# Optimization experiments

Hardware: AMD Instinct MI355X
Metric: run time of the kernel (lower is better)

Reference implementation:

```python
import jax, jax.numpy as jnp
import numpy as np
import math

B, N, CS, CZ, H, C, P, PV, NB = 1, 512, 384, 128, 12, 16, 4, 8, 64


def quat_to_rot(q):
    q = q / jnp.clip(jnp.linalg.norm(q, axis=-1, keepdims=True), 1e-8)
    w, x, y, z = q[..., 0], q[..., 1], q[..., 2], q[..., 3]
    return jnp.stack([
        w*w + x*x - y*y - z*z, 2*(x*y - w*z), 2*(x*z + w*y),
        2*(x*y + w*z), w*w - x*x + y*y - z*z, 2*(y*z - w*x),
        2*(x*z - w*y), 2*(y*z + w*x), w*w - x*x - y*y + z*z,
    ], axis=-1).reshape(q.shape[:-1] + (3, 3))


def setup_inputs() -> dict:
    key = jax.random.key(0)
    ks = jax.random.split(key, 28)
    def n(k, shape, sc=1.0):
        return jax.random.normal(k, shape, jnp.float32) * sc
    s = n(ks[0], (B, N, CS))
    z = n(ks[1], (B, N, N, CZ))
    translations = n(ks[2], (B, N, 3)) * 4.0  # spread distances over 0-32A bins
    rotations = quat_to_rot(n(ks[3], (B, N, 4)))  # valid SO(3) frames
    mask = jnp.ones((B, N), dtype=bool)
    inv = lambda fan: 1.0 / math.sqrt(fan)
    return {
        's': s, 'z': z, 'translations': translations, 'rotations': rotations, 'mask': mask,
        'Wq': n(ks[4], (CS, H*C), inv(CS)), 'bq': n(ks[5], (H*C,), 0.01),
        'Wk': n(ks[6], (CS, H*C), inv(CS)), 'bk': n(ks[7], (H*C,), 0.01),
        'Wv': n(ks[8], (CS, H*C), inv(CS)), 'bv': n(ks[9], (H*C,), 0.01),
        'Wqp': n(ks[10], (CS, H*P*3), inv(CS)), 'bqp': n(ks[11], (H*P*3,), 0.01),
        'Wkp': n(ks[12], (CS, H*P*3), inv(CS)), 'bkp': n(ks[13], (H*P*3,), 0.01),
        'Wvp': n(ks[14], (CS, H*PV*3), inv(CS)), 'bvp': n(ks[15], (H*PV*3,), 0.01),
        'Wb': n(ks[16], (CZ, H), inv(CZ)), 'bb': n(ks[17], (H,), 0.01),
        'dist_emb': n(ks[18], (NB, H), 0.02),
        'scale_logits': n(ks[19], (3, H), 0.1),
        'head_weights': jnp.abs(n(ks[20], (H,))) * 0.2 + 0.8,
        'Wout': n(ks[21], (H*(C + PV*4 + CZ), CS), inv(H*(C + PV*4 + CZ))),
        'bout': n(ks[22], (CS,), 0.01),
    }


def reference(s, z, translations, rotations, mask, Wq, bq, Wk, bk, Wv, bv,
              Wqp, bqp, Wkp, bkp, Wvp, bvp, Wb, bb, dist_emb, scale_logits,
              head_weights, Wout, bout):
    b, n, _ = s.shape
    q = (s @ Wq + bq).reshape(b, n, H, C)
    k = (s @ Wk + bk).reshape(b, n, H, C)
    v = (s @ Wv + bv).reshape(b, n, H, C)
    q_pts = (s @ Wqp + bqp).reshape(b, n, H, P, 3)
    k_pts = (s @ Wkp + bkp).reshape(b, n, H, P, 3)
    v_pts = (s @ Wvp + bvp).reshape(b, n, H, PV, 3)
    t = translations[:, :, None, None, :]
    q_g = jnp.einsum('bnij,bnhpj->bnhpi', rotations, q_pts) + t
    k_g = jnp.einsum('bnij,bnhpj->bnhpi', rotations, k_pts) + t
    v_g = jnp.einsum('bnij,bnhpj->bnhpi', rotations, v_pts) + t
    scalar_logits = jnp.einsum('bnhc,bmhc->bnmh', q, k) / math.sqrt(C)
    # squared point distances, summed over points p and coords i, via expansion
    q_sq = (q_g**2).sum((-1, -2))  # (b, n, h)
    k_sq = (k_g**2).sum((-1, -2))
    cross = jnp.einsum('bnhpi,bmhpi->bnmh', q_g, k_g)
    point_dist = q_sq[:, :, None, :] + k_sq[:, None, :, :] - 2.0 * cross
    point_logits = -0.5 * point_dist * head_weights
    pair_bias = z @ Wb + bb  # (b, n, m, h)
    pair_dist = jnp.linalg.norm(
        translations[:, :, None, :] - translations[:, None, :, :], axis=-1)
    edges = jnp.linspace(0.0, 32.0, NB + 1)
    bins = jnp.clip(jnp.searchsorted(edges, pair_dist, side='left') - 1, 0, NB - 1)
    dist_bias = dist_emb[bins]
    local = (pair_dist <= 5.0).astype(s.dtype)
    medium = ((pair_dist > 5.0) & (pair_dist <= 15.0)).astype(s.dtype)
    scales = jnp.stack([local, medium, jnp.ones_like(pair_dist)], axis=-1)
    per_head = jax.nn.softmax(scale_logits, axis=0)  # (3, h)
    multiscale = jnp.einsum('bnms,sh->bnmh', scales, per_head)
    logits = scalar_logits + point_logits + pair_bias + dist_bias + multiscale
    m2d = mask[:, :, None] & mask[:, None, :]
    logits = jnp.where(m2d[..., None], logits, -10000.0)
    attn = jax.nn.softmax(logits.astype(jnp.float32), axis=2).astype(s.dtype)
    out_scalar = jnp.einsum('bnmh,bmhc->bnhc', attn, v)
    out_pts_g = jnp.einsum('bnmh,bmhpi->bnhpi', attn, v_g)
    out_pts_l = jnp.einsum('bnji,bnhpj->bnhpi', rotations, out_pts_g - t)  # R^T x
    out_norms = jnp.linalg.norm(out_pts_l, axis=-1)  # (b, n, h, pv)
    pair_feat = jnp.einsum('bnmh,bnmc->bnhc', attn, z)
    feats = jnp.concatenate(
        [out_scalar, out_pts_l.reshape(b, n, H, PV * 3), out_norms, pair_feat],
        axis=-1).reshape(b, n, -1)
    return feats @ Wout + bout
```

## Files before the change

kernel.cpp:

```cpp
#include <hip/hip_runtime.h>
#include <math.h>

#define N   512
#define CS  384
#define CZ  128
#define H   12
#define C   16
#define P   4
#define PV  8
#define NB  64
#define KSP 528
#define QKD 28
#define QPAD 68
#define APAD 516
#define ZP2 132

#define OFF_Q    0
#define OFF_K    98304
#define OFF_V    196608
#define OFF_QP   294912
#define OFF_KP   368640
#define OFF_VP   442368
#define OFF_QG   589824
#define OFF_KG   663552
#define OFF_VG   737280
#define OFF_QSQ  884736
#define OFF_KSQ  890880
#define OFF_LOG  897024
#define OFF_FEAT 4042752

__global__ __launch_bounds__(256) void k_proj(
    const float* __restrict__ s,
    const float* __restrict__ Wq,  const float* __restrict__ bq,
    const float* __restrict__ Wk,  const float* __restrict__ bk,
    const float* __restrict__ Wv,  const float* __restrict__ bv,
    const float* __restrict__ Wqp, const float* __restrict__ bqp,
    const float* __restrict__ Wkp, const float* __restrict__ bkp,
    const float* __restrict__ Wvp, const float* __restrict__ bvp,
    float* __restrict__ ws)
{
    __shared__ float s_s[16*388];
    __shared__ float part[4*16*68];
    const int tid = threadIdx.x;
    const int n0  = blockIdx.y * 16;
    const int cq  = tid & 15;
    const int rg  = (tid >> 4) & 3;
    const int ks  = tid >> 6;
    const int gc  = blockIdx.x * 64 + cq * 4;
    for (int i = tid; i < 16*384; i += 256) {
        int r = i / 384, c = i - r*384;
        s_s[r*388 + c] = s[(n0 + r)*384 + c];
    }
    __syncthreads();
    const float* W; int width; int lc;
    if      (gc < 192) { W=Wq;  width=192; lc=gc;     }
    else if (gc < 384) { W=Wk;  width=192; lc=gc-192; }
    else if (gc < 576) { W=Wv;  width=192; lc=gc-384; }
    else if (gc < 720) { W=Wqp; width=144; lc=gc-576; }
    else if (gc < 864) { W=Wkp; width=144; lc=gc-720; }
    else               { W=Wvp; width=288; lc=gc-864; }
    float acc[4][4] = {{0.f}};
    const float* wp   = W + lc + (size_t)(ks*96)*width;
    const float* srow = s_s + (rg*4)*388 + ks*96;
    #pragma unroll 4
    for (int kk = 0; kk < 96; kk++) {
        float4 w4 = *(const float4*)(wp + (size_t)kk*width);
        #pragma unroll
        for (int r = 0; r < 4; r++) {
            float sv = srow[r*388 + kk];
            acc[r][0] += sv*w4.x; acc[r][1] += sv*w4.y;
            acc[r][2] += sv*w4.z; acc[r][3] += sv*w4.w;
        }
    }
    #pragma unroll
    for (int r = 0; r < 4; r++)
        *(float4*)(part + (ks*16 + rg*4 + r)*68 + cq*4) =
            make_float4(acc[r][0], acc[r][1], acc[r][2], acc[r][3]);
    __syncthreads();
    {
        const int row = tid >> 4;
        float4 sum = *(const float4*)(part + (0*16 + row)*68 + cq*4);
        #pragma unroll
        for (int k2 = 1; k2 < 4; k2++) {
            float4 p = *(const float4*)(part + (k2*16 + row)*68 + cq*4);
            sum.x += p.x; sum.y += p.y; sum.z += p.z; sum.w += p.w;
        }
        const float* b; float* dst; int w2, lc2;
        if      (gc < 192) { b=bq;  w2=192; lc2=gc;     dst=ws+OFF_Q;  }
        else if (gc < 384) { b=bk;  w2=192; lc2=gc-192; dst=ws+OFF_K;  }
        else if (gc < 576) { b=bv;  w2=192; lc2=gc-384; dst=ws+OFF_V;  }
        else if (gc < 720) { b=bqp; w2=144; lc2=gc-576; dst=ws+OFF_QP; }
        else if (gc < 864) { b=bkp; w2=144; lc2=gc-720; dst=ws+OFF_KP; }
        else               { b=bvp; w2=288; lc2=gc-864; dst=ws+OFF_VP; }
        float4 b4 = *(const float4*)(b + lc2);
        sum.x += b4.x; sum.y += b4.y; sum.z += b4.z; sum.w += b4.w;
        *(float4*)(dst + (size_t)(n0+row)*w2 + lc2) = sum;
    }
}

__global__ __launch_bounds__(192) void k_frames(
    const float* __restrict__ rot, const float* __restrict__ trans,
    const float* __restrict__ bout, float* __restrict__ out,
    float* __restrict__ ws)
{
    int n = blockIdx.x, tid = threadIdx.x;
    __shared__ float R[9], T[3], qg_s[144], kg_s[144];
    if (tid < 9) R[tid] = rot[n*9 + tid];
    if (tid < 3) T[tid] = trans[n*3 + tid];
    out[(size_t)n*CS + tid]       = bout[tid];
    out[(size_t)n*CS + 192 + tid] = bout[192 + tid];
    __syncthreads();
    if (tid < 48) {
        const float* lp = ws + OFF_QP + n*144 + tid*3;
        float l0=lp[0], l1=lp[1], l2=lp[2];
        float* gp = ws + OFF_QG + n*144 + tid*3;
        for (int i=0;i<3;i++){ float g = R[i*3+0]*l0 + R[i*3+1]*l1 + R[i*3+2]*l2 + T[i]; gp[i]=g; qg_s[tid*3+i]=g; }
    } else if (tid < 96) {
        int u = tid-48;
        const float* lp = ws + OFF_KP + n*144 + u*3;
        float l0=lp[0], l1=lp[1], l2=lp[2];
        float* gp = ws + OFF_KG + n*144 + u*3;
        for (int i=0;i<3;i++){ float g = R[i*3+0]*l0 + R[i*3+1]*l1 + R[i*3+2]*l2 + T[i]; gp[i]=g; kg_s[u*3+i]=g; }
    } else {
        int u = tid-96;
        const float* lp = ws + OFF_VP + n*288 + u*3;
        float l0=lp[0], l1=lp[1], l2=lp[2];
        float* gp = ws + OFF_VG + n*288 + u*3;
        for (int i=0;i<3;i++){ float g = R[i*3+0]*l0 + R[i*3+1]*l1 + R[i*3+2]*l2 + T[i]; gp[i]=g; }
    }
    __syncthreads();
    if (tid < 12) {
        float a=0;
        for (int d=0; d<12; d++){ float x=qg_s[tid*12+d]; a+=x*x; }
        ws[OFF_QSQ + n*12 + tid]=a;
    } else if (tid < 24) {
        int h = tid-12; float a=0;
        for (int d=0; d<12; d++){ float x=kg_s[h*12+d]; a+=x*x; }
        ws[OFF_KSQ + n*12 + h]=a;
    }
}

__global__ __launch_bounds__(256) void k_qkpt(
    const float* __restrict__ head_weights, float* __restrict__ ws)
{
    __shared__ float qs[QKD*QPAD], ks[QKD*QPAD], qa[64], kb[64];
    const int tid = threadIdx.x;
    const int m0 = blockIdx.x * 64, n0 = blockIdx.y * 64, h = blockIdx.z;
    const float hw = head_weights[h];
    for (int idx = tid; idx < 64*16; idx += 256) {
        int r = idx >> 4, c = idx & 15;
        qs[c*QPAD + r] = ws[OFF_Q + (n0+r)*192 + h*16 + c] * 0.25f;
        ks[c*QPAD + r] = ws[OFF_K + (m0+r)*192 + h*16 + c];
    }
    for (int idx = tid; idx < 64*12; idx += 256) {
        int r = idx / 12, c = idx % 12;
        qs[(16+c)*QPAD + r] = ws[OFF_QG + (n0+r)*144 + h*12 + c] * hw;
        ks[(16+c)*QPAD + r] = ws[OFF_KG + (m0+r)*144 + h*12 + c];
    }
    for (int idx = tid; idx < 64; idx += 256) {
        qa[idx] = -0.5f * hw * ws[OFF_QSQ + (n0+idx)*12 + h];
        kb[idx] = -0.5f * hw * ws[OFF_KSQ + (m0+idx)*12 + h];
    }
    __syncthreads();
    const int tx = tid & 15, ty = tid >> 4;
    float acc[4][4] = {{0.f}};
    #pragma unroll 4
    for (int d = 0; d < QKD; d++) {
        float4 a = *(const float4*)(qs + d*QPAD + ty*4);
        float4 b = *(const float4*)(ks + d*QPAD + tx*4);
        const float* ap = &a.x; const float* bp = &b.x;
        #pragma unroll
        for (int i=0;i<4;i++)
            #pragma unroll
            for (int j=0;j<4;j++) acc[i][j] += ap[i]*bp[j];
    }
    #pragma unroll
    for (int i=0;i<4;i++) {
        float ai = qa[ty*4+i];
        float4 r;
        r.x = acc[i][0] + ai + kb[tx*4+0];
        r.y = acc[i][1] + ai + kb[tx*4+1];
        r.z = acc[i][2] + ai + kb[tx*4+2];
        r.w = acc[i][3] + ai + kb[tx*4+3];
        *(float4*)(ws + OFF_LOG + ((size_t)(n0+ty*4+i)*H + h)*N + m0 + tx*4) = r;
    }
}

__global__ __launch_bounds__(256) void k_zbias2(
    const float* __restrict__ z, const float* __restrict__ trans,
    const float* __restrict__ Wb, const float* __restrict__ bb,
    const float* __restrict__ dist_emb, const float* __restrict__ scale_logits,
    float* __restrict__ ws)
{
    __shared__ float zs[64*ZP2];
    __shared__ float partial[4*64*13];
    __shared__ float Wb_s[CZ*12];
    __shared__ float sprob[36];
    const int mb = blockIdx.x, n = blockIdx.y;
    const int tid = threadIdx.x, lane = tid & 63, wave = tid >> 6;

    if (tid < 12) {
        float sa = scale_logits[tid], sb = scale_logits[12+tid], sc = scale_logits[24+tid];
        float mx = fmaxf(sa, fmaxf(sb, sc));
        float ea=__expf(sa-mx), eb=__expf(sb-mx), ec=__expf(sc-mx);
        float inv = 1.f/(ea+eb+ec);
        sprob[tid] = ea*inv; sprob[12+tid] = eb*inv; sprob[24+tid] = ec*inv;
    }
    for (int i = tid; i < 384; i += 256)
        *(float4*)(Wb_s + i*4) = *(const float4*)(Wb + i*4);
    __syncthreads();

    const float tnx = trans[n*3+0], tny = trans[n*3+1], tnz = trans[n*3+2];
    const int h0 = wave*3;

    for (int chunk = 0; chunk < 2; chunk++) {
        const int m0 = mb*128 + chunk*64;
        const float4* zsrc4 = (const float4*)(z + ((size_t)n*N + m0)*CZ);
        #pragma unroll
        for (int p = 0; p < 8; p++) {
            int idx = p*256 + tid;
            float4 v = zsrc4[idx];
            *(float4*)(zs + (idx>>5)*ZP2 + (idx&31)*4) = v;
        }
        __syncthreads();
        {
            const float* zrow = zs + lane*ZP2 + wave*32;
            float a[12];
            #pragma unroll
            for (int h=0;h<12;h++) a[h]=0.f;
            #pragma unroll
            for (int c4=0;c4<8;c4++) {
                float4 zq = *(const float4*)(zrow + c4*4);
                const float* wr = Wb_s + (wave*32 + c4*4)*12;
                const float* zp = &zq.x;
                #pragma unroll
                for (int j=0;j<4;j++) {
                    float4 w0 = *(const float4*)(wr + j*12);
                    float4 w1 = *(const float4*)(wr + j*12 + 4);
                    float4 w2 = *(const float4*)(wr + j*12 + 8);
                    float zj = zp[j];
                    a[0]+=zj*w0.x; a[1]+=zj*w0.y; a[2]+=zj*w0.z; a[3]+=zj*w0.w;
                    a[4]+=zj*w1.x; a[5]+=zj*w1.y; a[6]+=zj*w1.z; a[7]+=zj*w1.w;
                    a[8]+=zj*w2.x; a[9]+=zj*w2.y; a[10]+=zj*w2.z; a[11]+=zj*w2.w;
                }
            }
            float* pdst = partial + (wave*64 + lane)*13;
            #pragma unroll
            for (int h=0;h<12;h++) pdst[h] = a[h];
        }
        __syncthreads();
        {
            const int m = m0 + lane;
            float dx = tnx - trans[m*3+0];
            float dy = tny - trans[m*3+1];
            float dz = tnz - trans[m*3+2];
            float pdist = sqrtf(dx*dx+dy*dy+dz*dz);
            int bin = (int)ceilf(2.f*pdist) - 1;
            bin = bin < 0 ? 0 : (bin > NB-1 ? NB-1 : bin);
            const int ssel = (pdist <= 5.f) ? 0 : (pdist <= 15.f ? 1 : -1);
            float v0 = partial[(0*64+lane)*13 + h0]   + partial[(1*64+lane)*13 + h0]
                     + partial[(2*64+lane)*13 + h0]   + partial[(3*64+lane)*13 + h0];
            float v1 = partial[(0*64+lane)*13 + h0+1] + partial[(1*64+lane)*13 + h0+1]
                     + partial[(2*64+lane)*13 + h0+1] + partial[(3*64+lane)*13 + h0+1];
            float v2 = partial[(0*64+lane)*13 + h0+2] + partial[(1*64+lane)*13 + h0+2]
                     + partial[(2*64+lane)*13 + h0+2] + partial[(3*64+lane)*13 + h0+2];
            v0 += bb[h0]   + dist_emb[bin*12 + h0]   + sprob[24+h0];
            v1 += bb[h0+1] + dist_emb[bin*12 + h0+1] + sprob[24+h0+1];
            v2 += bb[h0+2] + dist_emb[bin*12 + h0+2] + sprob[24+h0+2];
            if (ssel == 0)      { v0 += sprob[h0];    v1 += sprob[h0+1];    v2 += sprob[h0+2]; }
            else if (ssel == 1) { v0 += sprob[12+h0]; v1 += sprob[12+h0+1]; v2 += sprob[12+h0+2]; }
            float* lp = ws + OFF_LOG + ((size_t)n*H + h0)*N + m;
            lp[0]   += v0;
            lp[N]   += v1;
            lp[2*N] += v2;
        }
        __syncthreads();
    }
}

__global__ __launch_bounds__(256) void k_attnmm(
    const float* __restrict__ z, const float* __restrict__ trans,
    const float* __restrict__ rot, float* __restrict__ ws)
{
    __shared__ float attn_s[H*APAD];
    __shared__ float part[4*12*64];
    __shared__ float og_s[288];
    const int n = blockIdx.x, role = blockIdx.y, tid = threadIdx.x;
    const int lane = tid & 63, wave = tid >> 6;

    const float4* asrc = (const float4*)(ws + OFF_LOG + (size_t)n*H*N);
    for (int i = tid; i < H*(N/4); i += 256) {
        int h = i >> 7, q = i & 127;
        *(float4*)(attn_s + h*APAD + q*4) = asrc[h*128 + q];
    }
    __syncthreads();
    for (int h = wave; h < H; h += 4) {
        float* row = attn_s + h*APAD;
        float v[8]; float mx = -1e30f;
        #pragma unroll
        for (int j=0;j<8;j++){ v[j]=row[lane + j*64]; mx = fmaxf(mx, v[j]); }
        #pragma unroll
        for (int off=32; off>0; off>>=1) mx = fmaxf(mx, __shfl_xor(mx, off, 64));
        float sum = 0.f;
        #pragma unroll
        for (int j=0;j<8;j++){ v[j]=__expf(v[j]-mx); sum += v[j]; }
        #pragma unroll
        for (int off=32; off>0; off>>=1) sum += __shfl_xor(sum, off, 64);
        float inv = 1.f/sum;
        #pragma unroll
        for (int j=0;j<8;j++) row[lane + j*64] = v[j]*inv;
    }
    __syncthreads();

    if (role == 0) {
        const int cq = tid & 15;
        const int ms = tid >> 4;
        for (int ch = 0; ch < 2; ch++) {
            const float* zb = z + (size_t)n*N*CZ + ch*64 + cq*4;
            float4 acc[12];
            #pragma unroll
            for (int h=0; h<12; h++) acc[h] = make_float4(0.f,0.f,0.f,0.f);
            const int r0 = ms*32;
            #pragma unroll 2
            for (int rq = 0; rq < 8; rq++) {
                const int r = r0 + rq*4;
                float4 z0 = *(const float4*)(zb + (size_t)(r+0)*CZ);
                float4 z1 = *(const float4*)(zb + (size_t)(r+1)*CZ);
                float4 z2 = *(const float4*)(zb + (size_t)(r+2)*CZ);
                float4 z3 = *(const float4*)(zb + (size_t)(r+3)*CZ);
                #pragma unroll
                for (int h=0; h<12; h++) {
                    float4 a4 = *(const float4*)(attn_s + h*APAD + r);
                    acc[h].x += a4.x*z0.x + a4.y*z1.x + a4.z*z2.x + a4.w*z3.x;
                    acc[h].y += a4.x*z0.y + a4.y*z1.y + a4.z*z2.y + a4.w*z3.y;
                    acc[h].z += a4.x*z0.z + a4.y*z1.z + a4.z*z2.z + a4.w*z3.z;
                    acc[h].w += a4.x*z0.w + a4.y*z1.w + a4.z*z2.w + a4.w*z3.w;
                }
            }
            #pragma unroll
            for (int h=0; h<12; h++) {
                acc[h].x += __shfl_xor(acc[h].x, 16, 64); acc[h].y += __shfl_xor(acc[h].y, 16, 64);
                acc[h].z += __shfl_xor(acc[h].z, 16, 64); acc[h].w += __shfl_xor(acc[h].w, 16, 64);
                acc[h].x += __shfl_xor(acc[h].x, 32, 64); acc[h].y += __shfl_xor(acc[h].y, 32, 64);
                acc[h].z += __shfl_xor(acc[h].z, 32, 64); acc[h].w += __shfl_xor(acc[h].w, 32, 64);
            }
            if (lane < 16) {
                #pragma unroll
                for (int h=0; h<12; h++)
                    *(float4*)(part + (wave*12 + h)*64 + lane*4) = acc[h];
            }
            __syncthreads();
            if (tid < 192) {
                const int h = tid >> 4, c4 = tid & 15;
                float4 s4 = *(const float4*)(part + (0*12 + h)*64 + c4*4);
                #pragma unroll
                for (int w=1; w<4; w++) {
                    float4 p = *(const float4*)(part + (w*12 + h)*64 + c4*4);
                    s4.x += p.x; s4.y += p.y; s4.z += p.z; s4.w += p.w;
                }
                *(float4*)(ws + OFF_FEAT + (size_t)n*2112 + h*176 + 48 + ch*64 + c4*4) = s4;
            }
            __syncthreads();
        }
    } else {
        if (tid < 240) {
            const int col4 = (tid % 120) * 4;
            const int msA  = tid / 120;
            const float* aptr; int astride, ah;
            if (col4 < 192) { ah = col4 >> 4;        aptr = ws + OFF_V  + col4;       astride = 192; }
            else            { ah = (col4-192) / 24;  aptr = ws + OFF_VG + (col4-192); astride = 288; }
            const float4* arow = (const float4*)(attn_s + ah*APAD);
            float4 acc = {0.f,0.f,0.f,0.f};
            #pragma unroll 2
            for (int mq = msA*64; mq < msA*64 + 64; mq++) {
                float4 a4 = arow[mq];
                const float* vp = aptr + (size_t)mq*4*astride;
                float4 v0 = *(const float4*)(vp);
                float4 v1 = *(const float4*)(vp + astride);
                float4 v2 = *(const float4*)(vp + 2*astride);
                float4 v3 = *(const float4*)(vp + 3*astride);
                acc.x += a4.x*v0.x + a4.y*v1.x + a4.z*v2.x + a4.w*v3.x;
                acc.y += a4.x*v0.y + a4.y*v1.y + a4.z*v2.y + a4.w*v3.y;
                acc.z += a4.x*v0.z + a4.y*v1.z + a4.z*v2.z + a4.w*v3.z;
                acc.w += a4.x*v0.w + a4.y*v1.w + a4.z*v2.w + a4.w*v3.w;
            }
            *(float4*)(part + tid*4) = acc;
        }
        __syncthreads();
        if (tid < 120) {
            const int col4 = tid * 4;
            float4 a = *(const float4*)(part + tid*4);
            float4 b = *(const float4*)(part + (tid+120)*4);
            a.x += b.x; a.y += b.y; a.z += b.z; a.w += b.w;
            if (col4 < 192) {
                const int ah = col4 >> 4;
                *(float4*)(ws + OFF_FEAT + (size_t)n*2112 + ah*176 + (col4 & 15)) = a;
            } else {
                *(float4*)(og_s + (col4 - 192)) = a;
            }
        }
        __syncthreads();
        if (tid < 96) {
            const int h = tid >> 3, p = tid & 7;
            float g0 = og_s[h*24 + p*3 + 0] - trans[n*3+0];
            float g1 = og_s[h*24 + p*3 + 1] - trans[n*3+1];
            float g2 = og_s[h*24 + p*3 + 2] - trans[n*3+2];
            const float* R = rot + n*9;
            float* fdst = ws + OFF_FEAT + (size_t)n*2112 + h*176;
            float nsq = 0.f;
            #pragma unroll
            for (int i=0;i<3;i++){
                float l = R[0*3+i]*g0 + R[1*3+i]*g1 + R[2*3+i]*g2;
                fdst[16 + p*3 + i] = l;
                nsq += l*l;
            }
            fdst[40 + p] = sqrtf(nsq);
        }
    }
}

__global__ __launch_bounds__(256) void k_out(
    const float* __restrict__ Wout, const float* __restrict__ ws,
    float* __restrict__ out)
{
    __shared__ float f_s[16*KSP];
    __shared__ float part[4*16*68];
    const int tid = threadIdx.x;
    const int n0  = blockIdx.y * 16;
    const int k0  = blockIdx.z * KSP;
    const int cq  = tid & 15;
    const int rg  = (tid >> 4) & 3;
    const int ks  = tid >> 6;
    const int col = blockIdx.x * 64 + cq * 4;
    for (int i = tid; i < 16*KSP; i += 256) {
        int r = i / KSP, c = i - r*KSP;
        f_s[i] = ws[OFF_FEAT + (size_t)(n0 + r)*2112 + k0 + c];
    }
    __syncthreads();
    float acc[4][4] = {{0.f}};
    const float* wp = Wout + (size_t)(k0 + ks*132)*CS + col;
    const float* f0 = f_s + (rg*4)*KSP + ks*132;
    #pragma unroll 4
    for (int kk = 0; kk < 132; kk++) {
        float4 w4 = *(const float4*)(wp + (size_t)kk*CS);
        #pragma unroll
        for (int r = 0; r < 4; r++) {
            float fv = f0[r*KSP + kk];
            acc[r][0] += fv*w4.x; acc[r][1] += fv*w4.y;
            acc[r][2] += fv*w4.z; acc[r][3] += fv*w4.w;
        }
    }
    #pragma unroll
    for (int r = 0; r < 4; r++)
        *(float4*)(part + (ks*16 + rg*4 + r)*68 + cq*4) =
            make_float4(acc[r][0], acc[r][1], acc[r][2], acc[r][3]);
    __syncthreads();
    {
        const int row = tid >> 4;
        float4 s = *(const float4*)(part + (0*16 + row)*68 + cq*4);
        #pragma unroll
        for (int k2 = 1; k2 < 4; k2++) {
            float4 p = *(const float4*)(part + (k2*16 + row)*68 + cq*4);
            s.x += p.x; s.y += p.y; s.z += p.z; s.w += p.w;
        }
        float* o = out + (size_t)(n0+row)*CS + col;
        atomicAdd(o+0, s.x); atomicAdd(o+1, s.y);
        atomicAdd(o+2, s.z); atomicAdd(o+3, s.w);
    }
}

extern "C" void kernel_launch(void* const* d_in, const int* in_sizes, int n_in,
                              void* d_out, int out_size, void* d_ws, size_t ws_size,
                              hipStream_t stream) {
    const float* s     = (const float*)d_in[0];
    const float* z     = (const float*)d_in[1];
    const float* trans = (const float*)d_in[2];
    const float* rot   = (const float*)d_in[3];
    const float* Wq  = (const float*)d_in[5];  const float* bq  = (const float*)d_in[6];
    const float* Wk  = (const float*)d_in[7];  const float* bk  = (const float*)d_in[8];
    const float* Wv  = (const float*)d_in[9];  const float* bv  = (const float*)d_in[10];
    const float* Wqp = (const float*)d_in[11]; const float* bqp = (const float*)d_in[12];
    const float* Wkp = (const float*)d_in[13]; const float* bkp = (const float*)d_in[14];
    const float* Wvp = (const float*)d_in[15]; const float* bvp = (const float*)d_in[16];
    const float* Wb  = (const float*)d_in[17]; const float* bb  = (const float*)d_in[18];
    const float* dist_emb     = (const float*)d_in[19];
    const float* scale_logits = (const float*)d_in[20];
    const float* head_weights = (const float*)d_in[21];
    const float* Wout = (const float*)d_in[22]; const float* bout = (const float*)d_in[23];
    float* out = (float*)d_out;
    float* ws  = (float*)d_ws;

    k_proj<<<dim3(18, 32), 256, 0, stream>>>(s, Wq,bq, Wk,bk, Wv,bv, Wqp,bqp, Wkp,bkp, Wvp,bvp, ws);
    k_frames<<<N, 192, 0, stream>>>(rot, trans, bout, out, ws);
    k_qkpt<<<dim3(8, 8, 12), 256, 0, stream>>>(head_weights, ws);
    k_zbias2<<<dim3(4, N), 256, 0, stream>>>(z, trans, Wb, bb, dist_emb, scale_logits, ws);
    k_attnmm<<<dim3(N, 2), 256, 0, stream>>>(z, trans, rot, ws);
    k_out<<<dim3(6, 32, 4), 256, 0, stream>>>(Wout, ws, out);
}
```

Measured before the change: 340.6 us.

## Merge attnmm roles into one 512-thread block per row, dropping cross-wave reductions

Replaces the two-block-per-row attention matmul (one block for pair features over z, one for value/point aggregation) with a single 512-thread block per row. The softmax is now computed once per row instead of twice. Each thread owns one (head, channel4) of the z contraction, or one full value column over all 512 keys, so the shared-memory partial buffers and the extra syncs for their reduction go away. In exchange each z-role thread runs a longer serial loop with fewer independent accumulators, and rows of z are re-read from global/L2 once per head.

```diff
diff --git a/kernel.cpp b/kernel.cpp
--- a/kernel.cpp
+++ b/kernel.cpp
@@ -278,23 +278,22 @@
     }
 }
 
-__global__ __launch_bounds__(256) void k_attnmm(
+__global__ __launch_bounds__(512, 2) void k_attnmm(
     const float* __restrict__ z, const float* __restrict__ trans,
     const float* __restrict__ rot, float* __restrict__ ws)
 {
     __shared__ float attn_s[H*APAD];
-    __shared__ float part[4*12*64];
     __shared__ float og_s[288];
-    const int n = blockIdx.x, role = blockIdx.y, tid = threadIdx.x;
+    const int n = blockIdx.x, tid = threadIdx.x;
     const int lane = tid & 63, wave = tid >> 6;
 
     const float4* asrc = (const float4*)(ws + OFF_LOG + (size_t)n*H*N);
-    for (int i = tid; i < H*(N/4); i += 256) {
+    for (int i = tid; i < H*(N/4); i += 512) {
         int h = i >> 7, q = i & 127;
         *(float4*)(attn_s + h*APAD + q*4) = asrc[h*128 + q];
     }
     __syncthreads();
-    for (int h = wave; h < H; h += 4) {
+    for (int h = wave; h < H; h += 8) {
         float* row = attn_s + h*APAD;
         float v[8]; float mx = -1e30f;
         #pragma unroll
@@ -312,110 +311,68 @@
     }
     __syncthreads();
 
-    if (role == 0) {
-        const int cq = tid & 15;
-        const int ms = tid >> 4;
-        for (int ch = 0; ch < 2; ch++) {
-            const float* zb = z + (size_t)n*N*CZ + ch*64 + cq*4;
-            float4 acc[12];
-            #pragma unroll
-            for (int h=0; h<12; h++) acc[h] = make_float4(0.f,0.f,0.f,0.f);
-            const int r0 = ms*32;
-            #pragma unroll 2
-            for (int rq = 0; rq < 8; rq++) {
-                const int r = r0 + rq*4;
-                float4 z0 = *(const float4*)(zb + (size_t)(r+0)*CZ);
-                float4 z1 = *(const float4*)(zb + (size_t)(r+1)*CZ);
-                float4 z2 = *(const float4*)(zb + (size_t)(r+2)*CZ);
-                float4 z3 = *(const float4*)(zb + (size_t)(r+3)*CZ);
-                #pragma unroll
-                for (int h=0; h<12; h++) {
-                    float4 a4 = *(const float4*)(attn_s + h*APAD + r);
-                    acc[h].x += a4.x*z0.x + a4.y*z1.x + a4.z*z2.x + a4.w*z3.x;
-                    acc[h].y += a4.x*z0.y + a4.y*z1.y + a4.z*z2.y + a4.w*z3.y;
-                    acc[h].z += a4.x*z0.z + a4.y*z1.z + a4.z*z2.z + a4.w*z3.z;
-                    acc[h].w += a4.x*z0.w + a4.y*z1.w + a4.z*z2.w + a4.w*z3.w;
-                }
-            }
-            #pragma unroll
-            for (int h=0; h<12; h++) {
-                acc[h].x += __shfl_xor(acc[h].x, 16, 64); acc[h].y += __shfl_xor(acc[h].y, 16, 64);
-                acc[h].z += __shfl_xor(acc[h].z, 16, 64); acc[h].w += __shfl_xor(acc[h].w, 16, 64);
-                acc[h].x += __shfl_xor(acc[h].x, 32, 64); acc[h].y += __shfl_xor(acc[h].y, 32, 64);
-                acc[h].z += __shfl_xor(acc[h].z, 32, 64); acc[h].w += __shfl_xor(acc[h].w, 32, 64);
-            }
-            if (lane < 16) {
-                #pragma unroll
-                for (int h=0; h<12; h++)
-                    *(float4*)(part + (wave*12 + h)*64 + lane*4) = acc[h];
-            }
-            __syncthreads();
-            if (tid < 192) {
-                const int h = tid >> 4, c4 = tid & 15;
-                float4 s4 = *(const float4*)(part + (0*12 + h)*64 + c4*4);
-                #pragma unroll
-                for (int w=1; w<4; w++) {
-                    float4 p = *(const float4*)(part + (w*12 + h)*64 + c4*4);
-                    s4.x += p.x; s4.y += p.y; s4.z += p.z; s4.w += p.w;
-                }
-                *(float4*)(ws + OFF_FEAT + (size_t)n*2112 + h*176 + 48 + ch*64 + c4*4) = s4;
-            }
-            __syncthreads();
-        }
-    } else {
-        if (tid < 240) {
-            const int col4 = (tid % 120) * 4;
-            const int msA  = tid / 120;
-            const float* aptr; int astride, ah;
-            if (col4 < 192) { ah = col4 >> 4;        aptr = ws + OFF_V  + col4;       astride = 192; }
-            else            { ah = (col4-192) / 24;  aptr = ws + OFF_VG + (col4-192); astride = 288; }
-            const float4* arow = (const float4*)(attn_s + ah*APAD);
-            float4 acc = {0.f,0.f,0.f,0.f};
-            #pragma unroll 2
-            for (int mq = msA*64; mq < msA*64 + 64; mq++) {
-                float4 a4 = arow[mq];
-                const float* vp = aptr + (size_t)mq*4*astride;
-                float4 v0 = *(const float4*)(vp);
-                float4 v1 = *(const float4*)(vp + astride);
-                float4 v2 = *(const float4*)(vp + 2*astride);
-                float4 v3 = *(const float4*)(vp + 3*astride);
-                acc.x += a4.x*v0.x + a4.y*v1.x + a4.z*v2.x + a4.w*v3.x;
-                acc.y += a4.x*v0.y + a4.y*v1.y + a4.z*v2.y + a4.w*v3.y;
-                acc.z += a4.x*v0.z + a4.y*v1.z + a4.z*v2.z + a4.w*v3.z;
-                acc.w += a4.x*v0.w + a4.y*v1.w + a4.z*v2.w + a4.w*v3.w;
-            }
-            *(float4*)(part + tid*4) = acc;
-        }
-        __syncthreads();
-        if (tid < 120) {
-            const int col4 = tid * 4;
-            float4 a = *(const float4*)(part + tid*4);
-            float4 b = *(const float4*)(part + (tid+120)*4);
-            a.x += b.x; a.y += b.y; a.z += b.z; a.w += b.w;
-            if (col4 < 192) {
-                const int ah = col4 >> 4;
-                *(float4*)(ws + OFF_FEAT + (size_t)n*2112 + ah*176 + (col4 & 15)) = a;
-            } else {
-                *(float4*)(og_s + (col4 - 192)) = a;
-            }
-        }
-        __syncthreads();
-        if (tid < 96) {
-            const int h = tid >> 3, p = tid & 7;
-            float g0 = og_s[h*24 + p*3 + 0] - trans[n*3+0];
-            float g1 = og_s[h*24 + p*3 + 1] - trans[n*3+1];
-            float g2 = og_s[h*24 + p*3 + 2] - trans[n*3+2];
-            const float* R = rot + n*9;
-            float* fdst = ws + OFF_FEAT + (size_t)n*2112 + h*176;
-            float nsq = 0.f;
-            #pragma unroll
-            for (int i=0;i<3;i++){
-                float l = R[0*3+i]*g0 + R[1*3+i]*g1 + R[2*3+i]*g2;
-                fdst[16 + p*3 + i] = l;
-                nsq += l*l;
-            }
-            fdst[40 + p] = sqrtf(nsq);
-        }
+    if (tid < 384) {
+        const int h  = tid >> 5;
+        const int c4 = tid & 31;
+        const float* zc   = z + (size_t)n*N*CZ + c4*4;
+        const float* arow = attn_s + h*APAD;
+        float4 acc = {0.f,0.f,0.f,0.f};
+        #pragma unroll 2
+        for (int m = 0; m < N; m += 4) {
+            float a0 = arow[m+0], a1 = arow[m+1], a2 = arow[m+2], a3 = arow[m+3];
+            float4 z0 = *(const float4*)(zc + (size_t)(m+0)*CZ);
+            float4 z1 = *(const float4*)(zc + (size_t)(m+1)*CZ);
+            float4 z2 = *(const float4*)(zc + (size_t)(m+2)*CZ);
+            float4 z3 = *(const float4*)(zc + (size_t)(m+3)*CZ);
+            acc.x += a0*z0.x + a1*z1.x + a2*z2.x + a3*z3.x;
+            acc.y += a0*z0.y + a1*z1.y + a2*z2.y + a3*z3.y;
+            acc.z += a0*z0.z + a1*z1.z + a2*z2.z + a3*z3.z;
+            acc.w += a0*z0.w + a1*z1.w + a2*z2.w + a3*z3.w;
+        }
+        *(float4*)(ws + OFF_FEAT + (size_t)n*2112 + h*176 + 48 + c4*4) = acc;
+    } else if (tid < 504) {
+        const int t = tid - 384;
+        const int col4 = t * 4;
+        const float* aptr; int astride, ah;
+        if (col4 < 192) { ah = col4 >> 4;        aptr = ws + OFF_V  + col4;       astride = 192; }
+        else            { ah = (col4-192) / 24;  aptr = ws + OFF_VG + (col4-192); astride = 288; }
+        const float4* arow = (const float4*)(attn_s + ah*APAD);
+        float4 acc = {0.f,0.f,0.f,0.f};
+        #pragma unroll 2
+        for (int mq = 0; mq < 128; mq++) {
+            float4 a4 = arow[mq];
+            const float* vp = aptr + (size_t)mq*4*astride;
+            float4 v0 = *(const float4*)(vp);
+            float4 v1 = *(const float4*)(vp + astride);
+            float4 v2 = *(const float4*)(vp + 2*astride);
+            float4 v3 = *(const float4*)(vp + 3*astride);
+            acc.x += a4.x*v0.x + a4.y*v1.x + a4.z*v2.x + a4.w*v3.x;
+            acc.y += a4.x*v0.y + a4.y*v1.y + a4.z*v2.y + a4.w*v3.y;
+            acc.z += a4.x*v0.z + a4.y*v1.z + a4.z*v2.z + a4.w*v3.z;
+            acc.w += a4.x*v0.w + a4.y*v1.w + a4.z*v2.w + a4.w*v3.w;
+        }
+        if (col4 < 192) {
+            *(float4*)(ws + OFF_FEAT + (size_t)n*2112 + (col4>>4)*176 + (col4&15)) = acc;
+        } else {
+            *(float4*)(og_s + (col4 - 192)) = acc;
+        }
+    }
+    __syncthreads();
+    if (tid < 96) {
+        const int h = tid >> 3, p = tid & 7;
+        float g0 = og_s[h*24 + p*3 + 0] - trans[n*3+0];
+        float g1 = og_s[h*24 + p*3 + 1] - trans[n*3+1];
+        float g2 = og_s[h*24 + p*3 + 2] - trans[n*3+2];
+        const float* R = rot + n*9;
+        float* fdst = ws + OFF_FEAT + (size_t)n*2112 + h*176;
+        float nsq = 0.f;
+        #pragma unroll
+        for (int i=0;i<3;i++){
+            float l = R[0*3+i]*g0 + R[1*3+i]*g1 + R[2*3+i]*g2;
+            fdst[16 + p*3 + i] = l;
+            nsq += l*l;
+        }
+        fdst[40 + p] = sqrtf(nsq);
     }
 }
 
@@ -494,6 +451,6 @@
     k_frames<<<N, 192, 0, stream>>>(rot, trans, bout, out, ws);
     k_qkpt<<<dim3(8, 8, 12), 256, 0, stream>>>(head_weights, ws);
     k_zbias2<<<dim3(4, N), 256, 0, stream>>>(z, trans, Wb, bb, dist_emb, scale_logits, ws);
-    k_attnmm<<<dim3(N, 2), 256, 0, stream>>>(z, trans, rot, ws);
+    k_attnmm<<<N, 512, 0, stream>>>(z, trans, rot, ws);
     k_out<<<dim3(6, 32, 4), 256, 0, stream>>>(Wout, ws, out);
 }
```

After: 372.5 us. 1.09x slower.
